# Performance work log

Measured on AMD Instinct MI355X. Metric: run time of the kernel, lower is better.

Reference implementation:

```python
import jax, jax.numpy as jnp
import numpy as np

B, N, IN_DIM, HID, OUT_DIM = 16, 1024, 128, 256, 1024
N_LAYERS, SCT_ORDER, GCN_ORDER = 2, 3, 1
TAU, N_ITER, NOISE_SCALE, TANH_SCALE = 0.1, 20, 0.05, 40.0


def _xavier(key, shape):
    # torch xavier_uniform_ on Linear weight [out, in]
    bound = np.sqrt(6.0 / (shape[-1] + shape[-2]))
    return jax.random.uniform(key, shape, jnp.float32, -bound, bound)


def setup_inputs() -> dict:
    key = jax.random.key(0)
    ks = jax.random.split(key, 12)
    L, H = N_LAYERS, HID
    return {
        "X": jax.random.normal(ks[0], (B, N, IN_DIM), jnp.float32),
        "adj": jax.random.uniform(ks[1], (B, N, N), jnp.float32),
        "w_in": _xavier(ks[2], (H, IN_DIM)),
        "b_in": jnp.zeros((H,), jnp.float32),
        "conv_w1": _xavier(ks[3], (L, H, H)),
        "conv_b1": jnp.zeros((L, H), jnp.float32),
        "conv_w2": _xavier(ks[4], (L, H, H)),
        "conv_b2": jnp.zeros((L, H), jnp.float32),
        "conv_a": 0.1 * jax.random.normal(ks[5], (L, 2 * H, 1), jnp.float32),
        "mlp1_w": _xavier(ks[6], (H, H * (1 + L))),
        "mlp1_b": jnp.zeros((H,), jnp.float32),
        "mlp2_w": _xavier(ks[7], (OUT_DIM, H)),
        "mlp2_b": jnp.zeros((OUT_DIM,), jnp.float32),
    }


def leaky(x):
    return jax.nn.leaky_relu(x, 0.01)


def gcn_diffusion(adj, order, X):
    eye = jnp.eye(adj.shape[-1], dtype=adj.dtype)
    A = adj + eye
    dis = A.sum(-1) ** -0.5                      # [B,N]
    A_hat = dis[..., :, None] * A * dis[..., None, :]
    outs, h = [], X
    for _ in range(order):
        h = A_hat @ h
        outs.append(h)
    return outs


def scattering_diffusion(adj, X, order):
    # lazy random walk P = (I + D^{-1} A)/2; wavelets psi_k = P^{2^{k-1}} - P^{2^k}
    Pmat = adj / adj.sum(-1, keepdims=True)

    def applyP(h):
        return 0.5 * (h + Pmat @ h)

    outs = []
    prev = X
    cur = applyP(X)
    outs.append(prev - cur)
    for k in range(2, order + 1):
        nxt = cur
        for _ in range(2 ** (k - 2)):
            nxt = applyP(nxt)
        outs.append(cur - nxt)
        cur = nxt
    return outs


def sct_conv(X, adj, w1, b1, w2, b2, a, moment=1):
    gcn_list = [leaky(g) for g in gcn_diffusion(adj, GCN_ORDER, X)]
    sct_list = [jnp.abs(h) ** moment for h in scattering_diffusion(adj, X, SCT_ORDER)]
    h_all = jnp.stack(gcn_list + sct_list, axis=1)                    # [B,C,N,H]
    x_rep = jnp.broadcast_to(X[:, None], h_all.shape)                 # [B,C,N,H]
    a_in = jnp.concatenate([x_rep, h_all], axis=-1)                   # [B,C,N,2H]
    e = (jax.nn.relu(a_in) @ a)[..., 0]                               # [B,C,N]
    attention = jax.nn.softmax(e + 1e-10, axis=1)[..., None]          # [B,C,N,1]
    h_prime = (attention * h_all).mean(axis=1)                        # [B,N,H]
    h = leaky(h_prime @ w1.T + b1)
    return leaky(h @ w2.T + b2)


def gumbel_sinkhorn(log_alpha, key):
    u = jax.random.uniform(key, log_alpha.shape, log_alpha.dtype)
    noise = -jnp.log(-jnp.log(u + 1e-20) + 1e-20) * NOISE_SCALE
    Z0 = (log_alpha + noise) / TAU

    def step(Z, _):
        Z = Z - jax.scipy.special.logsumexp(Z, axis=-1, keepdims=True)
        Z = Z - jax.scipy.special.logsumexp(Z, axis=-2, keepdims=True)
        return Z, None

    Z, _ = jax.lax.scan(step, Z0, None, length=N_ITER)
    P = jnp.exp(Z)
    P = P / P.sum(-1, keepdims=True)
    P = P / P.sum(-2, keepdims=True)
    return P, Z0


def reference(X, adj, w_in, b_in, conv_w1, conv_b1, conv_w2, conv_b2, conv_a,
              mlp1_w, mlp1_b, mlp2_w, mlp2_b):
    h = X @ w_in.T + b_in                                             # [B,N,H]
    hidden = [h]
    for l in range(N_LAYERS):
        h = sct_conv(h, adj, conv_w1[l], conv_b1[l], conv_w2[l], conv_b2[l], conv_a[l])
        hidden.append(h)
    h = jnp.concatenate(hidden, axis=-1)                              # [B,N,H*(1+L)]
    h = leaky(h @ mlp1_w.T + mlp1_b)
    logits = jnp.tanh(h @ mlp2_w.T + mlp2_b) * TANH_SCALE             # [B,N,N]
    P, gsinit = gumbel_sinkhorn(logits, jax.random.key(42))
    return P, gsinit
```

## Files before the change

kernel.cpp:

```cpp
#include <hip/hip_runtime.h>
#include <cstdint>
#include <cstddef>

#define BB 16
#define NN 1024
#define HD 256
#define IND 128
#define OUTD 1024
#define MROWS (BB*NN)

#define LEAKY(x) ((x) >= 0.0f ? (x) : 0.01f*(x))

typedef short short8 __attribute__((ext_vector_type(8)));
typedef float f32x4 __attribute__((ext_vector_type(4)));

#define GLL16(gsrc, ldst) __builtin_amdgcn_global_load_lds( \
    (const __attribute__((address_space(1))) unsigned int*)(gsrc), \
    (__attribute__((address_space(3))) unsigned int*)(ldst), 16, 0, 0)

#define CFENCE() asm volatile("" ::: "memory")

__device__ inline float wave_sum(float v){
  #pragma unroll
  for (int off=32; off; off>>=1) v += __shfl_xor(v, off, 64);
  return v;
}
__device__ inline float wave_max(float v){
  #pragma unroll
  for (int off=32; off; off>>=1) v = fmaxf(v, __shfl_xor(v, off, 64));
  return v;
}

__device__ inline unsigned short f2bf(float x){
  unsigned u = __float_as_uint(x);
  unsigned r = (u + 0x7fffu + ((u >> 16) & 1u)) >> 16;
  return (unsigned short)r;
}
__device__ inline float bf2f(unsigned short h){
  return __uint_as_float((unsigned)h << 16);
}

__device__ inline unsigned enc_e(float x){
  unsigned u = __float_as_uint(x);
  u += 0xFFFFFu + ((u>>20)&1u);
  int E = (int)(u>>23) - 112;
  if (E <= 0){
    unsigned Ms = (unsigned)__float2int_rn(x * 131072.0f);
    return (Ms >= 8u) ? 8u : Ms;
  }
  return ((unsigned)E<<3) | ((u>>20)&7u);
}
__device__ inline float dec_e(unsigned k){
  unsigned E = k>>3, M = k&7u;
  float nrm = __uint_as_float(((E+112u)<<23)|(M<<20));
  return E ? nrm : (float)M * 7.62939453125e-6f;
}

__device__ inline float gumbel_noise(unsigned m){
  const unsigned k0 = 0u, k1 = 42u;
  const unsigned ks2 = k0 ^ k1 ^ 0x1BD11BDAu;
  unsigned x0 = 0u, x1 = m;
  x0 += k0; x1 += k1;
  #define TF_ROUND(r) { x0 += x1; x1 = (x1 << (r)) | (x1 >> (32-(r))); x1 ^= x0; }
  TF_ROUND(13) TF_ROUND(15) TF_ROUND(26) TF_ROUND(6)
  x0 += k1;  x1 += ks2 + 1u;
  TF_ROUND(17) TF_ROUND(29) TF_ROUND(16) TF_ROUND(24)
  x0 += ks2; x1 += k0 + 2u;
  TF_ROUND(13) TF_ROUND(15) TF_ROUND(26) TF_ROUND(6)
  x0 += k0;  x1 += k1 + 3u;
  TF_ROUND(17) TF_ROUND(29) TF_ROUND(16) TF_ROUND(24)
  x0 += k1;  x1 += ks2 + 4u;
  TF_ROUND(13) TF_ROUND(15) TF_ROUND(26) TF_ROUND(6)
  x0 += ks2; x1 += k0 + 5u;
  #undef TF_ROUND
  unsigned bits = x0 ^ x1;
  float u = __uint_as_float((bits >> 9) | 0x3f800000u) - 1.0f;
  float t = -__logf(u + 1e-20f);
  return -__logf(t + 1e-20f) * 0.05f;
}

__global__ __launch_bounds__(256) void adj_prep_k(const float* __restrict__ adj,
                                                  float* __restrict__ dis,
                                                  float* __restrict__ rinv,
                                                  unsigned short* __restrict__ abf){
  int tid = threadIdx.x, wid = tid >> 6, lane = tid & 63;
  int row = blockIdx.x*4 + wid;
  const float4* rp = (const float4*)(adj + (size_t)row*NN);
  ushort4* op = (ushort4*)(abf + (size_t)row*NN);
  float s = 0.f;
  #pragma unroll
  for (int p=0;p<4;p++){
    float4 v = rp[lane + p*64];
    s += v.x+v.y+v.z+v.w;
    ushort4 o;
    o.x = f2bf(v.x); o.y = f2bf(v.y); o.z = f2bf(v.z); o.w = f2bf(v.w);
    op[lane + p*64] = o;
  }
  s = wave_sum(s);
  if (lane==0){
    dis[row]  = 1.0f/sqrtf(s + 1.0f);
    rinv[row] = 1.0f/s;
  }
}

__global__ __launch_bounds__(256) void split_flat_k(const float* __restrict__ src,
                                                    unsigned short* __restrict__ h,
                                                    unsigned short* __restrict__ l,
                                                    int n4){
  int gid = blockIdx.x*256 + threadIdx.x;
  if (gid >= n4) return;
  float4 v = ((const float4*)src)[gid];
  ushort4 hh, ll;
  hh.x = f2bf(v.x); ll.x = f2bf(v.x - bf2f(hh.x));
  hh.y = f2bf(v.y); ll.y = f2bf(v.y - bf2f(hh.y));
  hh.z = f2bf(v.z); ll.z = f2bf(v.z - bf2f(hh.z));
  hh.w = f2bf(v.w); ll.w = f2bf(v.w - bf2f(hh.w));
  ((ushort4*)h)[gid] = hh;
  ((ushort4*)l)[gid] = ll;
}

__global__ __launch_bounds__(256) void bconv_t_k(const float* __restrict__ in, int ld,
                                                 const float* __restrict__ scale,
                                                 unsigned short* __restrict__ outT){
  __shared__ float tile[64][68];
  int b  = blockIdx.z;
  int i0 = blockIdx.x*64;
  int c0 = blockIdx.y*64;
  const float* inb = in + (size_t)b*NN*ld;
  unsigned short* ob = outT + (size_t)b*HD*NN;
  int tid = threadIdx.x;
  #pragma unroll
  for (int it=0; it<4; it++){
    int f = tid + it*256;
    int r = f >> 4, c4 = (f & 15)*4;
    float4 v = *(const float4*)(inb + (size_t)(i0+r)*ld + c0 + c4);
    float s = scale ? scale[b*NN + i0 + r] : 1.0f;
    tile[r][c4+0]=v.x*s; tile[r][c4+1]=v.y*s; tile[r][c4+2]=v.z*s; tile[r][c4+3]=v.w*s;
  }
  __syncthreads();
  #pragma unroll
  for (int it=0; it<4; it++){
    int f = tid + it*256;
    int cl = f >> 4, r4 = (f & 15)*4;
    ushort4 o;
    o.x = f2bf(tile[r4+0][cl]);
    o.y = f2bf(tile[r4+1][cl]);
    o.z = f2bf(tile[r4+2][cl]);
    o.w = f2bf(tile[r4+3][cl]);
    *(ushort4*)(ob + (size_t)(c0+cl)*NN + i0 + r4) = o;
  }
}

__global__ __launch_bounds__(512) void gemm_nn_mfma_k(const unsigned short* __restrict__ Abf,
                                                      const unsigned short* __restrict__ Btb,
                                                      const float* __restrict__ Bsrc, int ldb,
                                                      const float* __restrict__ rowscale,
                                                      float* __restrict__ out,
                                                      float* __restrict__ out2,
                                                      const float* __restrict__ sub,
                                                      int mode){
  __shared__ unsigned short Als[2][128][32];
  __shared__ unsigned short Bls[2][128][32];
  int s = blockIdx.x + (blockIdx.y<<1) + (blockIdx.z<<4);
  int idx = (s&7)*32 + (s>>3);
  int b  = idx >> 4;
  int i0 = ((idx>>1)&7)*128;
  int n0 = (idx&1)*128;
  const unsigned short* Ab = Abf + (size_t)b*NN*NN + (size_t)i0*NN;
  const unsigned short* Bb = Btb + (size_t)b*HD*NN + (size_t)n0*NN;
  int tid = threadIdx.x;
  int wave = tid >> 6, lane = tid & 63;
  int quad = lane >> 4, l16 = lane & 15;
  int wr = (wave >> 2)*64;
  int wc = (wave & 3)*32;

  int r  = tid >> 2;
  int cg = (((tid & 3) ^ ((r >> 1) & 3)) << 3);
  int wbase = (tid >> 6) << 9;
  const unsigned short* gA = Ab + (size_t)r*NN + cg;
  const unsigned short* gB = Bb + (size_t)r*NN + cg;

  auto STAGE = [&](int c){
    int buf = c & 1;
    GLL16(gA + (c<<5), &Als[buf][0][0] + wbase);
    GLL16(gB + (c<<5), &Bls[buf][0][0] + wbase);
  };

  const int NC = NN/32;
  STAGE(0);

  f32x4 acc[4][2] = {};

  for (int c = 0; c < NC; ++c){
    if (c+1 < NC){
      STAGE(c+1);
      asm volatile("s_waitcnt vmcnt(2)" ::: "memory");
    } else {
      asm volatile("s_waitcnt vmcnt(0)" ::: "memory");
    }
    __builtin_amdgcn_s_barrier();
    CFENCE();
    int buf = c & 1;
    short8 af[4];
    #pragma unroll
    for (int rt=0; rt<4; rt++){
      int R = wr + rt*16 + l16;
      af[rt] = *(const short8*)&Als[buf][R][(quad ^ ((R >> 1) & 3)) << 3];
    }
    __builtin_amdgcn_s_setprio(1);
    #pragma unroll
    for (int ct=0; ct<2; ct++){
      int Rb = wc + ct*16 + l16;
      short8 bfr = *(const short8*)&Bls[buf][Rb][(quad ^ ((Rb >> 1) & 3)) << 3];
      #pragma unroll
      for (int rt=0; rt<4; rt++)
        acc[rt][ct] = __builtin_amdgcn_mfma_f32_16x16x32_bf16(af[rt], bfr, acc[rt][ct], 0, 0, 0);
    }
    __builtin_amdgcn_s_setprio(0);
    CFENCE();
    __builtin_amdgcn_s_barrier();
    CFENCE();
  }

  #pragma unroll
  for (int rt=0; rt<4; rt++){
    #pragma unroll
    for (int p=0; p<4; p++){
      int gr = i0 + wr + rt*16 + quad*4 + p;
      int gm = b*NN + gr;
      float sc = rowscale[gm];
      #pragma unroll
      for (int ct=0; ct<2; ct++){
        int gc = n0 + wc + ct*16 + l16;
        float a = acc[rt][ct][p];
        float src = Bsrc[(size_t)gm*ldb + gc];
        float o = (mode == 1) ? 0.5f*(src + sc*a) : LEAKY(sc*(a + sc*src));
        if (out) out[(size_t)gm*HD + gc] = o;
        if (out2){
          float sv = sub ? sub[(size_t)gm*HD + gc] : src;
          out2[(size_t)gm*HD + gc] = fabsf(sv - o);
        }
      }
    }
  }
}

__global__ __launch_bounds__(512) void gemm_nt_mfma_k(const unsigned short* __restrict__ Ah_,
                                                      const unsigned short* __restrict__ Al_,
                                                      int lda,
                                                      const unsigned short* __restrict__ Wh_,
                                                      const unsigned short* __restrict__ Wl_,
                                                      const float* __restrict__ bias,
                                                      float* __restrict__ out, int ldo,
                                                      unsigned short* __restrict__ outh,
                                                      unsigned short* __restrict__ outl,
                                                      int K, int act){
  __shared__ unsigned short AhL[2][128][32], AlL[2][128][32];
  __shared__ unsigned short WhL[2][128][32], WlL[2][128][32];
  int gx = gridDim.x;
  int sh = (gx == 2) ? 1 : 3;
  int s = blockIdx.x + blockIdx.y*gx;
  int nwg = gx*gridDim.y;
  int idx = (s&7)*(nwg>>3) + (s>>3);
  int o0 = (idx & (gx-1))*128;
  int m0 = (idx >> sh)*128;
  int tid = threadIdx.x;
  int wave = tid >> 6, lane = tid & 63;
  int quad = lane >> 4, l16 = lane & 15;
  int wr = (wave >> 2)*64;
  int wc = (wave & 3)*32;

  int r  = tid >> 2;
  int cg = (((tid & 3) ^ ((r >> 1) & 3)) << 3);
  int wbase = (tid >> 6) << 9;
  const unsigned short* gAh = Ah_ + (size_t)(m0 + r)*lda + cg;
  const unsigned short* gAl = Al_ + (size_t)(m0 + r)*lda + cg;
  const unsigned short* gWh = Wh_ + (size_t)(o0 + r)*K + cg;
  const unsigned short* gWl = Wl_ + (size_t)(o0 + r)*K + cg;

  int NC = K >> 5;

  auto STAGE = [&](int c){
    int buf = c & 1; int kc = c << 5;
    GLL16(gAh + kc, &AhL[buf][0][0] + wbase);
    GLL16(gAl + kc, &AlL[buf][0][0] + wbase);
    GLL16(gWh + kc, &WhL[buf][0][0] + wbase);
    GLL16(gWl + kc, &WlL[buf][0][0] + wbase);
  };

  STAGE(0);

  f32x4 acc[4][2] = {};

  for (int c = 0; c < NC; ++c){
    if (c+1 < NC){
      STAGE(c+1);
      asm volatile("s_waitcnt vmcnt(4)" ::: "memory");
    } else {
      asm volatile("s_waitcnt vmcnt(0)" ::: "memory");
    }
    __builtin_amdgcn_s_barrier();
    CFENCE();
    int buf = c & 1;
    short8 ah[4], al[4];
    #pragma unroll
    for (int rt=0; rt<4; rt++){
      int R = wr + rt*16 + l16;
      int sc = (quad ^ ((R >> 1) & 3)) << 3;
      ah[rt] = *(const short8*)&AhL[buf][R][sc];
      al[rt] = *(const short8*)&AlL[buf][R][sc];
    }
    __builtin_amdgcn_s_setprio(1);
    #pragma unroll
    for (int ct=0; ct<2; ct++){
      int Rb = wc + ct*16 + l16;
      int sc = (quad ^ ((Rb >> 1) & 3)) << 3;
      short8 wh = *(const short8*)&WhL[buf][Rb][sc];
      short8 wl = *(const short8*)&WlL[buf][Rb][sc];
      #pragma unroll
      for (int rt=0; rt<4; rt++){
        acc[rt][ct] = __builtin_amdgcn_mfma_f32_16x16x32_bf16(ah[rt], wh, acc[rt][ct], 0, 0, 0);
        acc[rt][ct] = __builtin_amdgcn_mfma_f32_16x16x32_bf16(al[rt], wh, acc[rt][ct], 0, 0, 0);
        acc[rt][ct] = __builtin_amdgcn_mfma_f32_16x16x32_bf16(ah[rt], wl, acc[rt][ct], 0, 0, 0);
      }
    }
    __builtin_amdgcn_s_setprio(0);
    CFENCE();
    __builtin_amdgcn_s_barrier();
    CFENCE();
  }

  #pragma unroll
  for (int rt=0; rt<4; rt++){
    #pragma unroll
    for (int p=0; p<4; p++){
      int gm = m0 + wr + rt*16 + quad*4 + p;
      #pragma unroll
      for (int ct=0; ct<2; ct++){
        int gc = o0 + wc + ct*16 + l16;
        float v = acc[rt][ct][p] + bias[gc];
        if (act == 1){
          v = LEAKY(v);
        } else if (act == 2){
          float vcl = fminf(fmaxf(v, -15.f), 15.f);
          float e = __expf(2.f*vcl);
          float lg = 40.0f * (e - 1.f) / (e + 1.f);
          unsigned flat = (unsigned)gm*1024u + (unsigned)gc;
          v = (lg + gumbel_noise(flat)) / 0.1f;
        }
        if (out) out[(size_t)gm*ldo + gc] = v;
        if (outh){
          unsigned short hh = f2bf(v);
          outh[(size_t)gm*ldo + gc] = hh;
          outl[(size_t)gm*ldo + gc] = f2bf(v - bf2f(hh));
        }
      }
    }
  }
}

__global__ __launch_bounds__(256) void attn_k(const float* __restrict__ c0,
                                              const float* __restrict__ s0,
                                              const float* __restrict__ s1,
                                              const float* __restrict__ s2,
                                              const float* __restrict__ a2,
                                              unsigned short* __restrict__ outh,
                                              unsigned short* __restrict__ outl){
  int tid = threadIdx.x, wid = tid >> 6, lane = tid & 63;
  int row = blockIdx.x*4 + wid;
  size_t base = (size_t)row*HD + lane*4;
  float4 av = *(const float4*)(a2 + lane*4);
  float4 v[4];
  v[0] = *(const float4*)(c0 + base);
  v[1] = *(const float4*)(s0 + base);
  v[2] = *(const float4*)(s1 + base);
  v[3] = *(const float4*)(s2 + base);
  float e[4];
  #pragma unroll
  for (int c=0;c<4;c++){
    float p = fmaxf(v[c].x,0.f)*av.x + fmaxf(v[c].y,0.f)*av.y
            + fmaxf(v[c].z,0.f)*av.z + fmaxf(v[c].w,0.f)*av.w;
    e[c] = wave_sum(p);
  }
  float m = fmaxf(fmaxf(e[0],e[1]), fmaxf(e[2],e[3]));
  float w0 = expf(e[0]-m), w1 = expf(e[1]-m), w2 = expf(e[2]-m), w3 = expf(e[3]-m);
  float inv = 0.25f / (w0+w1+w2+w3);
  float4 o;
  o.x = (w0*v[0].x + w1*v[1].x + w2*v[2].x + w3*v[3].x)*inv;
  o.y = (w0*v[0].y + w1*v[1].y + w2*v[2].y + w3*v[3].y)*inv;
  o.z = (w0*v[0].z + w1*v[1].z + w2*v[2].z + w3*v[3].z)*inv;
  o.w = (w0*v[0].w + w1*v[1].w + w2*v[2].w + w3*v[3].w)*inv;
  ushort4 oh, ol;
  oh.x = f2bf(o.x); ol.x = f2bf(o.x - bf2f(oh.x));
  oh.y = f2bf(o.y); ol.y = f2bf(o.y - bf2f(oh.y));
  oh.z = f2bf(o.z); ol.z = f2bf(o.z - bf2f(oh.z));
  oh.w = f2bf(o.w); ol.w = f2bf(o.w - bf2f(oh.w));
  *(ushort4*)(outh + base) = oh;
  *(ushort4*)(outl + base) = ol;
}

__global__ __launch_bounds__(256) void rowmax_k(const float* __restrict__ Z,
                                                float* __restrict__ alpha){
  int tid = threadIdx.x, wid = tid >> 6, lane = tid & 63;
  int row = blockIdx.x*4 + wid;
  const float4* rp = (const float4*)(Z + (size_t)row*NN);
  float m = -3.4e38f;
  #pragma unroll
  for (int p=0;p<4;p++){
    float4 v = rp[lane + p*64];
    m = fmaxf(m, fmaxf(fmaxf(v.x,v.y), fmaxf(v.z,v.w)));
  }
  m = wave_max(m);
  if (lane==0) alpha[row] = m;
}

__global__ __launch_bounds__(256) void colmax_k(const float* __restrict__ Z,
                                                const float* __restrict__ alpha,
                                                float* __restrict__ pmax){
  int b = blockIdx.y, rc = blockIdx.x;
  int j = threadIdx.x*4;
  const float* Zb = Z + (size_t)b*NN*NN;
  const float* ab = alpha + b*NN;
  float4 m = make_float4(-3.4e38f,-3.4e38f,-3.4e38f,-3.4e38f);
  int r0 = rc*32;
  #pragma unroll 4
  for (int r=r0; r<r0+32; r++){
    float4 v = *(const float4*)(Zb + (size_t)r*NN + j);
    float a = ab[r];
    m.x = fmaxf(m.x, v.x-a); m.y = fmaxf(m.y, v.y-a);
    m.z = fmaxf(m.z, v.z-a); m.w = fmaxf(m.w, v.w-a);
  }
  *(float4*)(pmax + ((size_t)b*32 + rc)*NN + j) = m;
}

__global__ __launch_bounds__(256) void colred_k(const float* __restrict__ pmax,
                                                float* __restrict__ beta){
  int b = blockIdx.y;
  int j = blockIdx.x*256 + threadIdx.x;
  float m = -3.4e38f;
  #pragma unroll
  for (int rc=0; rc<32; rc++)
    m = fmaxf(m, pmax[((size_t)b*32+rc)*NN + j]);
  beta[b*NN + j] = m;
}

__global__ __launch_bounds__(256) void build_e_k(const float* __restrict__ Z,
                                                 const float* __restrict__ alpha,
                                                 const float* __restrict__ beta,
                                                 unsigned char* __restrict__ E,
                                                 unsigned char* __restrict__ Et){
  __shared__ float tile[64][65];
  int b = blockIdx.z;
  int i0 = blockIdx.y*64, j0 = blockIdx.x*64;
  const float* Zb = Z + (size_t)b*NN*NN;
  const float* ab = alpha + b*NN;
  const float* bb = beta  + b*NN;
  unsigned char* Eb  = E  + (size_t)b*NN*NN;
  unsigned char* Etb = Et + (size_t)b*NN*NN;
  int tid = threadIdx.x;
  #pragma unroll
  for (int it=0; it<4; it++){
    int f = tid + it*256;
    int r = f >> 4, c4 = (f & 15)*4;
    float4 v = *(const float4*)(Zb + (size_t)(i0+r)*NN + j0 + c4);
    float a = ab[i0+r];
    float e0 = __expf(v.x - a - bb[j0+c4+0]);
    float e1 = __expf(v.y - a - bb[j0+c4+1]);
    float e2 = __expf(v.z - a - bb[j0+c4+2]);
    float e3 = __expf(v.w - a - bb[j0+c4+3]);
    tile[r][c4+0]=e0; tile[r][c4+1]=e1; tile[r][c4+2]=e2; tile[r][c4+3]=e3;
    uchar4 o;
    o.x=(unsigned char)enc_e(e0); o.y=(unsigned char)enc_e(e1);
    o.z=(unsigned char)enc_e(e2); o.w=(unsigned char)enc_e(e3);
    *(uchar4*)(Eb + (size_t)(i0+r)*NN + j0 + c4) = o;
  }
  __syncthreads();
  #pragma unroll
  for (int it=0; it<4; it++){
    int f = tid + it*256;
    int r = f >> 4, c4 = (f & 15)*4;
    uchar4 o;
    o.x = (unsigned char)enc_e(tile[c4+0][r]);
    o.y = (unsigned char)enc_e(tile[c4+1][r]);
    o.z = (unsigned char)enc_e(tile[c4+2][r]);
    o.w = (unsigned char)enc_e(tile[c4+3][r]);
    *(uchar4*)(Etb + (size_t)(j0+r)*NN + i0 + c4) = o;
  }
}

__global__ __launch_bounds__(256) void mv_k(const unsigned char* __restrict__ M,
                                            const float* __restrict__ v,
                                            float* __restrict__ w, int recip){
  int tid = threadIdx.x, wid = tid >> 6, lane = tid & 63;
  int row = blockIdx.x*4 + wid;
  int b = row >> 10;
  uint4 mw = *((const uint4*)(M + (size_t)row*NN) + lane);
  float s = 0.f;
  if (v){
    const float* vb = v + b*NN + lane*16;
    float4 v0 = *(const float4*)(vb);
    float4 v1 = *(const float4*)(vb+4);
    float4 v2 = *(const float4*)(vb+8);
    float4 v3 = *(const float4*)(vb+12);
    s += dec_e(mw.x&255u)*v0.x + dec_e((mw.x>>8)&255u)*v0.y
       + dec_e((mw.x>>16)&255u)*v0.z + dec_e(mw.x>>24)*v0.w;
    s += dec_e(mw.y&255u)*v1.x + dec_e((mw.y>>8)&255u)*v1.y
       + dec_e((mw.y>>16)&255u)*v1.z + dec_e(mw.y>>24)*v1.w;
    s += dec_e(mw.z&255u)*v2.x + dec_e((mw.z>>8)&255u)*v2.y
       + dec_e((mw.z>>16)&255u)*v2.z + dec_e(mw.z>>24)*v2.w;
    s += dec_e(mw.w&255u)*v3.x + dec_e((mw.w>>8)&255u)*v3.y
       + dec_e((mw.w>>16)&255u)*v3.z + dec_e(mw.w>>24)*v3.w;
  } else {
    s += dec_e(mw.x&255u) + dec_e((mw.x>>8)&255u) + dec_e((mw.x>>16)&255u) + dec_e(mw.x>>24);
    s += dec_e(mw.y&255u) + dec_e((mw.y>>8)&255u) + dec_e((mw.y>>16)&255u) + dec_e(mw.y>>24);
    s += dec_e(mw.z&255u) + dec_e((mw.z>>8)&255u) + dec_e((mw.z>>16)&255u) + dec_e(mw.z>>24);
    s += dec_e(mw.w&255u) + dec_e((mw.w>>8)&255u) + dec_e((mw.w>>16)&255u) + dec_e(mw.w>>24);
  }
  s = wave_sum(s);
  if (lane==0) w[row] = recip ? 1.0f/s : s;
}

__global__ __launch_bounds__(256) void writep_lin_k(const unsigned char* __restrict__ E,
                                                    const float* __restrict__ ap,
                                                    const float* __restrict__ tp,
                                                    float* __restrict__ P){
  int gid = blockIdx.x*256 + threadIdx.x;
  int row = gid >> 8;
  int j = (gid & 255)*4;
  int b = row >> 10;
  uchar4 e = ((const uchar4*)E)[gid];
  float a = ap[row];
  float4 t = *(const float4*)(tp + (size_t)b*NN + j);
  float4 o;
  o.x = dec_e(e.x)*a/t.x;
  o.y = dec_e(e.y)*a/t.y;
  o.z = dec_e(e.z)*a/t.z;
  o.w = dec_e(e.w)*a/t.w;
  ((float4*)P)[gid] = o;
}

extern "C" void kernel_launch(void* const* d_in, const int* in_sizes, int n_in,
                              void* d_out, int out_size, void* d_ws, size_t ws_size,
                              hipStream_t stream){
  const float* X    = (const float*)d_in[0];
  const float* adj  = (const float*)d_in[1];
  const float* w_in = (const float*)d_in[2];
  const float* b_in = (const float*)d_in[3];
  const float* cw1  = (const float*)d_in[4];
  const float* cb1  = (const float*)d_in[5];
  const float* cw2  = (const float*)d_in[6];
  const float* cb2  = (const float*)d_in[7];
  const float* ca   = (const float*)d_in[8];
  const float* m1w  = (const float*)d_in[9];
  const float* m1b  = (const float*)d_in[10];
  const float* m2w  = (const float*)d_in[11];
  const float* m2b  = (const float*)d_in[12];

  float* outp = (float*)d_out;
  float* Pout = outp;
  float* Z0   = outp + (size_t)16*1024*1024;

  const size_t SLOT = (size_t)4*1024*1024;
  float* s1 = outp + 0*SLOT;
  float* s2 = outp + 1*SLOT;
  float* s3 = outp + 2*SLOT;
  float* s4 = outp + 3*SLOT;
  float* s5 = outp + 4*SLOT;
  unsigned short* adjbf = (unsigned short*)(outp + 6*SLOT);

  unsigned short* Xh  = (unsigned short*)(outp + 0*SLOT);
  unsigned short* Xl  = Xh + (size_t)MROWS*IND;
  unsigned short* s4h = (unsigned short*)(outp + 3*SLOT);
  unsigned short* s4l = s4h + (size_t)MROWS*HD;
  unsigned short* l1h = (unsigned short*)(outp + 0*SLOT);
  unsigned short* l1l = l1h + (size_t)MROWS*HD;
  unsigned short* m1sh = (unsigned short*)(outp + 1*SLOT);
  unsigned short* m1sl = m1sh + (size_t)MROWS*HD;
  unsigned short* Hh = (unsigned short*)(outp + 2*SLOT);
  unsigned short* Hl = Hh + (size_t)MROWS*768;
  float* alpha = s1;
  float* beta  = s1 + 16384;
  float* pmaxb = s1 + 32768;

  float* ws     = (float*)d_ws;
  float* hidden = ws;
  float* dis    = ws + (size_t)12*1024*1024;
  float* rinv   = dis + 16384;
  unsigned short* bt = (unsigned short*)(rinv + 16384);
  unsigned short* wsp = (unsigned short*)(ws + (size_t)15*1024*1024);
  unsigned short* winh = wsp;               unsigned short* winl = winh + 32768;
  unsigned short* w1h  = winl + 32768;      unsigned short* w1l  = w1h + 131072;
  unsigned short* w2h  = w1l + 131072;      unsigned short* w2l  = w2h + 131072;
  unsigned short* m1h  = w2l + 131072;      unsigned short* m1l  = m1h + 196608;
  unsigned short* m2h  = m1l + 196608;      unsigned short* m2l  = m2h + 262144;
  unsigned char* E  = (unsigned char*)ws;
  unsigned char* Et = E + (size_t)MROWS*NN;
  float* av = ws + (size_t)16*1024*1024;
  float* bv = av + 16384;
  float* tv = bv + 16384;

  dim3 blk(256);
  dim3 gEw(4096);
  dim3 gMM(2, 8, 16);
  dim3 gCT(16, 4, 16);

  adj_prep_k<<<gEw, blk, 0, stream>>>(adj, dis, rinv, adjbf);
  split_flat_k<<<dim3(32),  blk, 0, stream>>>(w_in, winh, winl, 8192);
  split_flat_k<<<dim3(128), blk, 0, stream>>>(cw1,  w1h,  w1l,  32768);
  split_flat_k<<<dim3(128), blk, 0, stream>>>(cw2,  w2h,  w2l,  32768);
  split_flat_k<<<dim3(192), blk, 0, stream>>>(m1w,  m1h,  m1l,  49152);
  split_flat_k<<<dim3(256), blk, 0, stream>>>(m2w,  m2h,  m2l,  65536);
  split_flat_k<<<dim3(2048), blk, 0, stream>>>(X, Xh, Xl, 524288);

  gemm_nt_mfma_k<<<dim3(2,128), dim3(512), 0, stream>>>(Xh, Xl, IND,
                                                        winh, winl, b_in,
                                                        hidden, 768, nullptr, nullptr,
                                                        IND, 0);

  for (int l=0; l<2; l++){
    const float* h_in = hidden + l*HD;
    unsigned short* wl1h = w1h + (size_t)l*65536;
    unsigned short* wl1l = w1l + (size_t)l*65536;
    unsigned short* wl2h = w2h + (size_t)l*65536;
    unsigned short* wl2l = w2l + (size_t)l*65536;
    const float* b1 = cb1 + (size_t)l*HD;
    const float* b2 = cb2 + (size_t)l*HD;
    const float* a2 = ca  + (size_t)l*2*HD + HD;

    bconv_t_k<<<gCT, blk, 0, stream>>>(h_in, 768, dis, bt);
    gemm_nn_mfma_k<<<gMM, dim3(512), 0, stream>>>(adjbf, bt, h_in, 768, dis, s2, nullptr, nullptr, 2);
    bconv_t_k<<<gCT, blk, 0, stream>>>(h_in, 768, nullptr, bt);
    gemm_nn_mfma_k<<<gMM, dim3(512), 0, stream>>>(adjbf, bt, h_in, 768, rinv, s1, s3, nullptr, 1);
    bconv_t_k<<<gCT, blk, 0, stream>>>(s1, HD, nullptr, bt);
    gemm_nn_mfma_k<<<gMM, dim3(512), 0, stream>>>(adjbf, bt, s1, HD, rinv, s4, s5, nullptr, 1);
    bconv_t_k<<<gCT, blk, 0, stream>>>(s4, HD, nullptr, bt);
    gemm_nn_mfma_k<<<gMM, dim3(512), 0, stream>>>(adjbf, bt, s4, HD, rinv, s1, nullptr, nullptr, 1);
    bconv_t_k<<<gCT, blk, 0, stream>>>(s1, HD, nullptr, bt);
    gemm_nn_mfma_k<<<gMM, dim3(512), 0, stream>>>(adjbf, bt, s1, HD, rinv, nullptr, s1, s4, 1);
    attn_k<<<gEw, blk, 0, stream>>>(s2, s3, s5, s1, a2, s4h, s4l);
    gemm_nt_mfma_k<<<dim3(2,128), dim3(512), 0, stream>>>(s4h, s4l, HD,
                                                          wl1h, wl1l, b1,
                                                          nullptr, HD, l1h, l1l,
                                                          HD, 1);
    gemm_nt_mfma_k<<<dim3(2,128), dim3(512), 0, stream>>>(l1h, l1l, HD,
                                                          wl2h, wl2l, b2,
                                                          hidden + (l+1)*HD, 768,
                                                          nullptr, nullptr, HD, 1);
  }

  split_flat_k<<<dim3(12288), blk, 0, stream>>>(hidden, Hh, Hl, 3145728);
  gemm_nt_mfma_k<<<dim3(2,128), dim3(512), 0, stream>>>(Hh, Hl, 768,
                                                        m1h, m1l, m1b,
                                                        nullptr, HD, m1sh, m1sl,
                                                        768, 1);
  gemm_nt_mfma_k<<<dim3(8,128), dim3(512), 0, stream>>>(m1sh, m1sl, HD,
                                                        m2h, m2l, m2b,
                                                        Z0, OUTD, nullptr, nullptr,
                                                        HD, 2);

  rowmax_k<<<gEw, blk, 0, stream>>>(Z0, alpha);
  colmax_k<<<dim3(32,16), blk, 0, stream>>>(Z0, alpha, pmaxb);
  colred_k<<<dim3(4,16), blk, 0, stream>>>(pmaxb, beta);
  build_e_k<<<dim3(16,16,16), blk, 0, stream>>>(Z0, alpha, beta, E, Et);

  mv_k<<<gEw, blk, 0, stream>>>(E,  nullptr, av, 1);
  mv_k<<<gEw, blk, 0, stream>>>(Et, av,      bv, 1);
  for (int t=1; t<20; t++){
    mv_k<<<gEw, blk, 0, stream>>>(E,  bv, av, 1);
    mv_k<<<gEw, blk, 0, stream>>>(Et, av, bv, 1);
  }
  mv_k<<<gEw, blk, 0, stream>>>(E,  bv, av, 1);
  mv_k<<<gEw, blk, 0, stream>>>(Et, av, tv, 0);
  writep_lin_k<<<dim3(16384), blk, 0, stream>>>(E, av, tv, Pout);
}
```

Baseline: 1.216 ms.

## Fuse Sinkhorn iterations into persistent kernel with grid barrier; deepen GEMM pipeline

```diff
diff --git a/kernel.cpp b/kernel.cpp
--- a/kernel.cpp
+++ b/kernel.cpp
@@ -8,6 +8,7 @@
 #define IND 128
 #define OUTD 1024
 #define MROWS (BB*NN)
+#define NBLK 256
 
 #define LEAKY(x) ((x) >= 0.0f ? (x) : 0.01f*(x))
 
@@ -42,18 +43,31 @@
 
 __device__ inline unsigned enc_e(float x){
   unsigned u = __float_as_uint(x);
-  u += 0xFFFFFu + ((u>>20)&1u);
-  int E = (int)(u>>23) - 112;
-  if (E <= 0){
-    unsigned Ms = (unsigned)__float2int_rn(x * 131072.0f);
-    return (Ms >= 8u) ? 8u : Ms;
-  }
-  return ((unsigned)E<<3) | ((u>>20)&7u);
+  u += 0x7FFFFu + ((u>>20)&1u);
+  unsigned e = u>>23;
+  if (e < 97u) return 0u;
+  return ((e-96u)<<3) | ((u>>20)&7u);
 }
 __device__ inline float dec_e(unsigned k){
-  unsigned E = k>>3, M = k&7u;
-  float nrm = __uint_as_float(((E+112u)<<23)|(M<<20));
-  return E ? nrm : (float)M * 7.62939453125e-6f;
+  float nrm = __uint_as_float((k + 768u) << 20);
+  return k ? nrm : 0.0f;
+}
+
+__device__ inline void gsync(unsigned* bar){
+  asm volatile("s_waitcnt vmcnt(0)" ::: "memory");
+  __syncthreads();
+  if (threadIdx.x == 0){
+    unsigned g = __hip_atomic_load(&bar[1], __ATOMIC_RELAXED, __HIP_MEMORY_SCOPE_AGENT);
+    unsigned o = __hip_atomic_fetch_add(&bar[0], 1u, __ATOMIC_RELAXED, __HIP_MEMORY_SCOPE_AGENT);
+    if (o == NBLK-1u){
+      __hip_atomic_store(&bar[0], 0u, __ATOMIC_RELAXED, __HIP_MEMORY_SCOPE_AGENT);
+      __hip_atomic_fetch_add(&bar[1], 1u, __ATOMIC_RELEASE, __HIP_MEMORY_SCOPE_AGENT);
+    } else {
+      while (__hip_atomic_load(&bar[1], __ATOMIC_RELAXED, __HIP_MEMORY_SCOPE_AGENT) == g)
+        __builtin_amdgcn_s_sleep(16);
+    }
+  }
+  __syncthreads();
 }
 
 __device__ inline float gumbel_noise(unsigned m){
@@ -159,8 +173,8 @@
                                                       float* __restrict__ out2,
                                                       const float* __restrict__ sub,
                                                       int mode){
-  __shared__ unsigned short Als[2][128][32];
-  __shared__ unsigned short Bls[2][128][32];
+  __shared__ unsigned short Als[4][128][32];
+  __shared__ unsigned short Bls[4][128][32];
   int s = blockIdx.x + (blockIdx.y<<1) + (blockIdx.z<<4);
   int idx = (s&7)*32 + (s>>3);
   int b  = idx >> 4;
@@ -180,27 +194,29 @@
   const unsigned short* gA = Ab + (size_t)r*NN + cg;
   const unsigned short* gB = Bb + (size_t)r*NN + cg;
 
-  auto STAGE = [&](int c){
-    int buf = c & 1;
-    GLL16(gA + (c<<5), &Als[buf][0][0] + wbase);
-    GLL16(gB + (c<<5), &Bls[buf][0][0] + wbase);
+  auto STAGE = [&](int t){
+    int buf = t & 3;
+    GLL16(gA + (t<<5), &Als[buf][0][0] + wbase);
+    GLL16(gB + (t<<5), &Bls[buf][0][0] + wbase);
   };
 
-  const int NC = NN/32;
-  STAGE(0);
+  const int NT = NN/32;
+  STAGE(0); STAGE(1);
 
   f32x4 acc[4][2] = {};
 
-  for (int c = 0; c < NC; ++c){
-    if (c+1 < NC){
-      STAGE(c+1);
+  for (int t = 0; t < NT; ++t){
+    if (t+2 < NT){
+      STAGE(t+2);
+      asm volatile("s_waitcnt vmcnt(4)" ::: "memory");
+    } else if (t+1 < NT){
       asm volatile("s_waitcnt vmcnt(2)" ::: "memory");
     } else {
       asm volatile("s_waitcnt vmcnt(0)" ::: "memory");
     }
     __builtin_amdgcn_s_barrier();
     CFENCE();
-    int buf = c & 1;
+    int buf = t & 3;
     short8 af[4];
     #pragma unroll
     for (int rt=0; rt<4; rt++){
@@ -217,9 +233,6 @@
         acc[rt][ct] = __builtin_amdgcn_mfma_f32_16x16x32_bf16(af[rt], bfr, acc[rt][ct], 0, 0, 0);
     }
     __builtin_amdgcn_s_setprio(0);
-    CFENCE();
-    __builtin_amdgcn_s_barrier();
-    CFENCE();
   }
 
   #pragma unroll
@@ -399,38 +412,37 @@
   *(ushort4*)(outl + base) = ol;
 }
 
-__global__ __launch_bounds__(256) void rowmax_k(const float* __restrict__ Z,
-                                                float* __restrict__ alpha){
+__global__ __launch_bounds__(256) void rowcolmax_k(const float* __restrict__ Z,
+                                                   float* __restrict__ alpha,
+                                                   float* __restrict__ pmax){
+  __shared__ float al[64];
   int tid = threadIdx.x, wid = tid >> 6, lane = tid & 63;
-  int row = blockIdx.x*4 + wid;
-  const float4* rp = (const float4*)(Z + (size_t)row*NN);
-  float m = -3.4e38f;
-  #pragma unroll
-  for (int p=0;p<4;p++){
-    float4 v = rp[lane + p*64];
-    m = fmaxf(m, fmaxf(fmaxf(v.x,v.y), fmaxf(v.z,v.w)));
-  }
-  m = wave_max(m);
-  if (lane==0) alpha[row] = m;
-}
-
-__global__ __launch_bounds__(256) void colmax_k(const float* __restrict__ Z,
-                                                const float* __restrict__ alpha,
-                                                float* __restrict__ pmax){
-  int b = blockIdx.y, rc = blockIdx.x;
-  int j = threadIdx.x*4;
-  const float* Zb = Z + (size_t)b*NN*NN;
-  const float* ab = alpha + b*NN;
-  float4 m = make_float4(-3.4e38f,-3.4e38f,-3.4e38f,-3.4e38f);
-  int r0 = rc*32;
+  int blk = blockIdx.x;
+  int r0 = blk << 6;
+  #pragma unroll 1
+  for (int rr=0; rr<16; ++rr){
+    int lr = (wid<<4) + rr;
+    const float4* rp = (const float4*)(Z + ((size_t)(r0+lr)<<10));
+    float m = -3.4e38f;
+    #pragma unroll
+    for (int p4=0;p4<4;p4++){
+      float4 v = rp[lane + p4*64];
+      m = fmaxf(m, fmaxf(fmaxf(v.x,v.y), fmaxf(v.z,v.w)));
+    }
+    m = wave_max(m);
+    if (lane==0){ al[lr] = m; alpha[r0+lr] = m; }
+  }
+  __syncthreads();
+  int j = tid*4;
+  float4 mm = make_float4(-3.4e38f,-3.4e38f,-3.4e38f,-3.4e38f);
   #pragma unroll 4
-  for (int r=r0; r<r0+32; r++){
-    float4 v = *(const float4*)(Zb + (size_t)r*NN + j);
-    float a = ab[r];
-    m.x = fmaxf(m.x, v.x-a); m.y = fmaxf(m.y, v.y-a);
-    m.z = fmaxf(m.z, v.z-a); m.w = fmaxf(m.w, v.w-a);
-  }
-  *(float4*)(pmax + ((size_t)b*32 + rc)*NN + j) = m;
+  for (int rr=0; rr<64; ++rr){
+    float4 v = *(const float4*)(Z + ((size_t)(r0+rr)<<10) + j);
+    float a = al[rr];
+    mm.x = fmaxf(mm.x, v.x-a); mm.y = fmaxf(mm.y, v.y-a);
+    mm.z = fmaxf(mm.z, v.z-a); mm.w = fmaxf(mm.w, v.w-a);
+  }
+  *(float4*)(pmax + ((size_t)blk<<10) + j) = mm;
 }
 
 __global__ __launch_bounds__(256) void colred_k(const float* __restrict__ pmax,
@@ -439,8 +451,8 @@
   int j = blockIdx.x*256 + threadIdx.x;
   float m = -3.4e38f;
   #pragma unroll
-  for (int rc=0; rc<32; rc++)
-    m = fmaxf(m, pmax[((size_t)b*32+rc)*NN + j]);
+  for (int rc=0; rc<16; rc++)
+    m = fmaxf(m, pmax[((size_t)(b*16+rc)<<10) + j]);
   beta[b*NN + j] = m;
 }
 
@@ -488,55 +500,87 @@
   }
 }
 
-__global__ __launch_bounds__(256) void mv_k(const unsigned char* __restrict__ M,
-                                            const float* __restrict__ v,
-                                            float* __restrict__ w, int recip){
+__global__ __launch_bounds__(256, 1) void sinkhorn_pers_k(const unsigned char* __restrict__ E,
+                                                          const unsigned char* __restrict__ Et,
+                                                          float* __restrict__ av,
+                                                          float* __restrict__ bv,
+                                                          float* __restrict__ tv,
+                                                          unsigned* __restrict__ bar,
+                                                          float* __restrict__ P){
   int tid = threadIdx.x, wid = tid >> 6, lane = tid & 63;
-  int row = blockIdx.x*4 + wid;
-  int b = row >> 10;
-  uint4 mw = *((const uint4*)(M + (size_t)row*NN) + lane);
-  float s = 0.f;
-  if (v){
-    const float* vb = v + b*NN + lane*16;
-    float4 v0 = *(const float4*)(vb);
-    float4 v1 = *(const float4*)(vb+4);
-    float4 v2 = *(const float4*)(vb+8);
-    float4 v3 = *(const float4*)(vb+12);
-    s += dec_e(mw.x&255u)*v0.x + dec_e((mw.x>>8)&255u)*v0.y
-       + dec_e((mw.x>>16)&255u)*v0.z + dec_e(mw.x>>24)*v0.w;
-    s += dec_e(mw.y&255u)*v1.x + dec_e((mw.y>>8)&255u)*v1.y
-       + dec_e((mw.y>>16)&255u)*v1.z + dec_e(mw.y>>24)*v1.w;
-    s += dec_e(mw.z&255u)*v2.x + dec_e((mw.z>>8)&255u)*v2.y
-       + dec_e((mw.z>>16)&255u)*v2.z + dec_e(mw.z>>24)*v2.w;
-    s += dec_e(mw.w&255u)*v3.x + dec_e((mw.w>>8)&255u)*v3.y
-       + dec_e((mw.w>>16)&255u)*v3.z + dec_e(mw.w>>24)*v3.w;
-  } else {
-    s += dec_e(mw.x&255u) + dec_e((mw.x>>8)&255u) + dec_e((mw.x>>16)&255u) + dec_e(mw.x>>24);
-    s += dec_e(mw.y&255u) + dec_e((mw.y>>8)&255u) + dec_e((mw.y>>16)&255u) + dec_e(mw.y>>24);
-    s += dec_e(mw.z&255u) + dec_e((mw.z>>8)&255u) + dec_e((mw.z>>16)&255u) + dec_e(mw.z>>24);
-    s += dec_e(mw.w&255u) + dec_e((mw.w>>8)&255u) + dec_e((mw.w>>16)&255u) + dec_e(mw.w>>24);
-  }
-  s = wave_sum(s);
-  if (lane==0) w[row] = recip ? 1.0f/s : s;
-}
-
-__global__ __launch_bounds__(256) void writep_lin_k(const unsigned char* __restrict__ E,
-                                                    const float* __restrict__ ap,
-                                                    const float* __restrict__ tp,
-                                                    float* __restrict__ P){
-  int gid = blockIdx.x*256 + threadIdx.x;
-  int row = gid >> 8;
-  int j = (gid & 255)*4;
-  int b = row >> 10;
-  uchar4 e = ((const uchar4*)E)[gid];
-  float a = ap[row];
-  float4 t = *(const float4*)(tp + (size_t)b*NN + j);
-  float4 o;
-  o.x = dec_e(e.x)*a/t.x;
-  o.y = dec_e(e.y)*a/t.y;
-  o.z = dec_e(e.z)*a/t.z;
-  o.w = dec_e(e.w)*a/t.w;
-  ((float4*)P)[gid] = o;
+  int blk = blockIdx.x;
+  int r0 = blk << 6;
+  int vbase = (r0 >> 10) << 10;
+
+  float vreg[16];
+  #pragma unroll
+  for (int q=0;q<16;q++) vreg[q] = 1.0f;
+
+  #define DECSUM(mwp, base) ( \
+      dec_e( (mwp)      &255u)*vreg[base+0] + dec_e(((mwp)>>8 )&255u)*vreg[base+1] + \
+      dec_e(((mwp)>>16) &255u)*vreg[base+2] + dec_e( (mwp)>>24       )*vreg[base+3] )
+
+  for (int p = 0; p < 42; ++p){
+    const unsigned char* M = (p & 1) ? Et : E;
+    float* wout = (p & 1) ? ((p == 41) ? tv : bv) : av;
+    int recip = (p != 41);
+    #pragma unroll 1
+    for (int rr=0; rr<16; ++rr){
+      int row = r0 + (wid<<4) + rr;
+      uint4 mw = *((const uint4*)(M + ((size_t)row<<10)) + lane);
+      float s = DECSUM(mw.x,0) + DECSUM(mw.y,4) + DECSUM(mw.z,8) + DECSUM(mw.w,12);
+      s = wave_sum(s);
+      if (lane==0){
+        float o = recip ? 1.0f/s : s;
+        __hip_atomic_store(&wout[row], o, __ATOMIC_RELAXED, __HIP_MEMORY_SCOPE_AGENT);
+      }
+    }
+    gsync(bar);
+    if (p < 41){
+      const float* vin = (p & 1) ? bv : av;
+      #pragma unroll
+      for (int q=0;q<16;q++)
+        vreg[q] = __hip_atomic_load(&vin[vbase + lane*16 + q],
+                                    __ATOMIC_RELAXED, __HIP_MEMORY_SCOPE_AGENT);
+    }
+  }
+  #undef DECSUM
+
+  float tinv[16];
+  #pragma unroll
+  for (int q=0;q<16;q++){
+    float t = __hip_atomic_load(&tv[vbase + lane*16 + q],
+                                __ATOMIC_RELAXED, __HIP_MEMORY_SCOPE_AGENT);
+    tinv[q] = 1.0f/t;
+  }
+  #pragma unroll 1
+  for (int rr=0; rr<16; ++rr){
+    int row = r0 + (wid<<4) + rr;
+    float a = __hip_atomic_load(&av[row], __ATOMIC_RELAXED, __HIP_MEMORY_SCOPE_AGENT);
+    uint4 mw = *((const uint4*)(E + ((size_t)row<<10)) + lane);
+    float* Pr = P + ((size_t)row<<10) + lane*16;
+    float4 o;
+    o.x = dec_e( mw.x      &255u)*a*tinv[0];
+    o.y = dec_e((mw.x>>8 ) &255u)*a*tinv[1];
+    o.z = dec_e((mw.x>>16) &255u)*a*tinv[2];
+    o.w = dec_e( mw.x>>24        )*a*tinv[3];
+    *(float4*)(Pr+0) = o;
+    o.x = dec_e( mw.y      &255u)*a*tinv[4];
+    o.y = dec_e((mw.y>>8 ) &255u)*a*tinv[5];
+    o.z = dec_e((mw.y>>16) &255u)*a*tinv[6];
+    o.w = dec_e( mw.y>>24        )*a*tinv[7];
+    *(float4*)(Pr+4) = o;
+    o.x = dec_e( mw.z      &255u)*a*tinv[8];
+    o.y = dec_e((mw.z>>8 ) &255u)*a*tinv[9];
+    o.z = dec_e((mw.z>>16) &255u)*a*tinv[10];
+    o.w = dec_e( mw.z>>24        )*a*tinv[11];
+    *(float4*)(Pr+8) = o;
+    o.x = dec_e( mw.w      &255u)*a*tinv[12];
+    o.y = dec_e((mw.w>>8 ) &255u)*a*tinv[13];
+    o.z = dec_e((mw.w>>16) &255u)*a*tinv[14];
+    o.w = dec_e( mw.w>>24        )*a*tinv[15];
+    *(float4*)(Pr+12) = o;
+  }
 }
 
 extern "C" void kernel_launch(void* const* d_in, const int* in_sizes, int n_in,
@@ -598,6 +642,7 @@
   float* av = ws + (size_t)16*1024*1024;
   float* bv = av + 16384;
   float* tv = bv + 16384;
+  unsigned* bar = (unsigned*)(tv + 16384);
 
   dim3 blk(256);
   dim3 gEw(4096);
@@ -658,18 +703,9 @@
                                                         Z0, OUTD, nullptr, nullptr,
                                                         HD, 2);
 
-  rowmax_k<<<gEw, blk, 0, stream>>>(Z0, alpha);
-  colmax_k<<<dim3(32,16), blk, 0, stream>>>(Z0, alpha, pmaxb);
+  rowcolmax_k<<<dim3(256), blk, 0, stream>>>(Z0, alpha, pmaxb);
   colred_k<<<dim3(4,16), blk, 0, stream>>>(pmaxb, beta);
   build_e_k<<<dim3(16,16,16), blk, 0, stream>>>(Z0, alpha, beta, E, Et);
-
-  mv_k<<<gEw, blk, 0, stream>>>(E,  nullptr, av, 1);
-  mv_k<<<gEw, blk, 0, stream>>>(Et, av,      bv, 1);
-  for (int t=1; t<20; t++){
-    mv_k<<<gEw, blk, 0, stream>>>(E,  bv, av, 1);
-    mv_k<<<gEw, blk, 0, stream>>>(Et, av, bv, 1);
-  }
-  mv_k<<<gEw, blk, 0, stream>>>(E,  bv, av, 1);
-  mv_k<<<gEw, blk, 0, stream>>>(Et, av, tv, 0);
-  writep_lin_k<<<dim3(16384), blk, 0, stream>>>(E, av, tv, Pout);
-}
+  hipMemsetAsync(bar, 0, 2*sizeof(unsigned), stream);
+  sinkhorn_pers_k<<<dim3(NBLK), blk, 0, stream>>>(E, Et, av, bv, tv, bar, Pout);
+}
```

New measurement: 1.773 ms. +45.8%, slower.

## Deepen GEMM prefetch, fuse transpose conversions and row/col max, change E encoding

Applied to the files above, without the earlier changes.

```diff
diff --git a/kernel.cpp b/kernel.cpp
--- a/kernel.cpp
+++ b/kernel.cpp
@@ -42,18 +42,14 @@
 
 __device__ inline unsigned enc_e(float x){
   unsigned u = __float_as_uint(x);
-  u += 0xFFFFFu + ((u>>20)&1u);
-  int E = (int)(u>>23) - 112;
-  if (E <= 0){
-    unsigned Ms = (unsigned)__float2int_rn(x * 131072.0f);
-    return (Ms >= 8u) ? 8u : Ms;
-  }
-  return ((unsigned)E<<3) | ((u>>20)&7u);
+  u += 0x7FFFFu + ((u>>20)&1u);
+  unsigned e = u>>23;
+  if (e < 97u) return 0u;
+  return ((e-96u)<<3) | ((u>>20)&7u);
 }
 __device__ inline float dec_e(unsigned k){
-  unsigned E = k>>3, M = k&7u;
-  float nrm = __uint_as_float(((E+112u)<<23)|(M<<20));
-  return E ? nrm : (float)M * 7.62939453125e-6f;
+  float nrm = __uint_as_float((k + 768u) << 20);
+  return k ? nrm : 0.0f;
 }
 
 __device__ inline float gumbel_noise(unsigned m){
@@ -151,6 +147,44 @@
   }
 }
 
+__global__ __launch_bounds__(256) void bconv2_t_k(const float* __restrict__ in, int ld,
+                                                  const float* __restrict__ scale,
+                                                  unsigned short* __restrict__ outS,
+                                                  unsigned short* __restrict__ outP){
+  __shared__ float tile[64][68];
+  __shared__ float srow[64];
+  int b  = blockIdx.z;
+  int i0 = blockIdx.x*64;
+  int c0 = blockIdx.y*64;
+  const float* inb = in + (size_t)b*NN*ld;
+  unsigned short* obS = outS + (size_t)b*HD*NN;
+  unsigned short* obP = outP + (size_t)b*HD*NN;
+  int tid = threadIdx.x;
+  if (tid < 64) srow[tid] = scale[b*NN + i0 + tid];
+  #pragma unroll
+  for (int it=0; it<4; it++){
+    int f = tid + it*256;
+    int r = f >> 4, c4 = (f & 15)*4;
+    float4 v = *(const float4*)(inb + (size_t)(i0+r)*ld + c0 + c4);
+    tile[r][c4+0]=v.x; tile[r][c4+1]=v.y; tile[r][c4+2]=v.z; tile[r][c4+3]=v.w;
+  }
+  __syncthreads();
+  #pragma unroll
+  for (int it=0; it<4; it++){
+    int f = tid + it*256;
+    int cl = f >> 4, r4 = (f & 15)*4;
+    float t0 = tile[r4+0][cl], t1 = tile[r4+1][cl];
+    float t2 = tile[r4+2][cl], t3 = tile[r4+3][cl];
+    ushort4 p, s;
+    p.x = f2bf(t0); p.y = f2bf(t1); p.z = f2bf(t2); p.w = f2bf(t3);
+    s.x = f2bf(t0*srow[r4+0]); s.y = f2bf(t1*srow[r4+1]);
+    s.z = f2bf(t2*srow[r4+2]); s.w = f2bf(t3*srow[r4+3]);
+    size_t off = (size_t)(c0+cl)*NN + i0 + r4;
+    *(ushort4*)(obP + off) = p;
+    *(ushort4*)(obS + off) = s;
+  }
+}
+
 __global__ __launch_bounds__(512) void gemm_nn_mfma_k(const unsigned short* __restrict__ Abf,
                                                       const unsigned short* __restrict__ Btb,
                                                       const float* __restrict__ Bsrc, int ldb,
@@ -159,8 +193,8 @@
                                                       float* __restrict__ out2,
                                                       const float* __restrict__ sub,
                                                       int mode){
-  __shared__ unsigned short Als[2][128][32];
-  __shared__ unsigned short Bls[2][128][32];
+  __shared__ unsigned short Als[4][128][32];
+  __shared__ unsigned short Bls[4][128][32];
   int s = blockIdx.x + (blockIdx.y<<1) + (blockIdx.z<<4);
   int idx = (s&7)*32 + (s>>3);
   int b  = idx >> 4;
@@ -180,27 +214,29 @@
   const unsigned short* gA = Ab + (size_t)r*NN + cg;
   const unsigned short* gB = Bb + (size_t)r*NN + cg;
 
-  auto STAGE = [&](int c){
-    int buf = c & 1;
-    GLL16(gA + (c<<5), &Als[buf][0][0] + wbase);
-    GLL16(gB + (c<<5), &Bls[buf][0][0] + wbase);
+  auto STAGE = [&](int t){
+    int buf = t & 3;
+    GLL16(gA + (t<<5), &Als[buf][0][0] + wbase);
+    GLL16(gB + (t<<5), &Bls[buf][0][0] + wbase);
   };
 
-  const int NC = NN/32;
-  STAGE(0);
+  const int NT = NN/32;
+  STAGE(0); STAGE(1);
 
   f32x4 acc[4][2] = {};
 
-  for (int c = 0; c < NC; ++c){
-    if (c+1 < NC){
-      STAGE(c+1);
+  for (int t = 0; t < NT; ++t){
+    if (t+2 < NT){
+      STAGE(t+2);
+      asm volatile("s_waitcnt vmcnt(4)" ::: "memory");
+    } else if (t+1 < NT){
       asm volatile("s_waitcnt vmcnt(2)" ::: "memory");
     } else {
       asm volatile("s_waitcnt vmcnt(0)" ::: "memory");
     }
     __builtin_amdgcn_s_barrier();
     CFENCE();
-    int buf = c & 1;
+    int buf = t & 3;
     short8 af[4];
     #pragma unroll
     for (int rt=0; rt<4; rt++){
@@ -217,9 +253,6 @@
         acc[rt][ct] = __builtin_amdgcn_mfma_f32_16x16x32_bf16(af[rt], bfr, acc[rt][ct], 0, 0, 0);
     }
     __builtin_amdgcn_s_setprio(0);
-    CFENCE();
-    __builtin_amdgcn_s_barrier();
-    CFENCE();
   }
 
   #pragma unroll
@@ -399,38 +432,37 @@
   *(ushort4*)(outl + base) = ol;
 }
 
-__global__ __launch_bounds__(256) void rowmax_k(const float* __restrict__ Z,
-                                                float* __restrict__ alpha){
+__global__ __launch_bounds__(256) void rowcolmax_k(const float* __restrict__ Z,
+                                                   float* __restrict__ alpha,
+                                                   float* __restrict__ pmax){
+  __shared__ float al[64];
   int tid = threadIdx.x, wid = tid >> 6, lane = tid & 63;
-  int row = blockIdx.x*4 + wid;
-  const float4* rp = (const float4*)(Z + (size_t)row*NN);
-  float m = -3.4e38f;
-  #pragma unroll
-  for (int p=0;p<4;p++){
-    float4 v = rp[lane + p*64];
-    m = fmaxf(m, fmaxf(fmaxf(v.x,v.y), fmaxf(v.z,v.w)));
-  }
-  m = wave_max(m);
-  if (lane==0) alpha[row] = m;
-}
-
-__global__ __launch_bounds__(256) void colmax_k(const float* __restrict__ Z,
-                                                const float* __restrict__ alpha,
-                                                float* __restrict__ pmax){
-  int b = blockIdx.y, rc = blockIdx.x;
-  int j = threadIdx.x*4;
-  const float* Zb = Z + (size_t)b*NN*NN;
-  const float* ab = alpha + b*NN;
-  float4 m = make_float4(-3.4e38f,-3.4e38f,-3.4e38f,-3.4e38f);
-  int r0 = rc*32;
+  int blk = blockIdx.x;
+  int r0 = blk << 6;
+  #pragma unroll 1
+  for (int rr=0; rr<16; ++rr){
+    int lr = (wid<<4) + rr;
+    const float4* rp = (const float4*)(Z + ((size_t)(r0+lr)<<10));
+    float m = -3.4e38f;
+    #pragma unroll
+    for (int p4=0;p4<4;p4++){
+      float4 v = rp[lane + p4*64];
+      m = fmaxf(m, fmaxf(fmaxf(v.x,v.y), fmaxf(v.z,v.w)));
+    }
+    m = wave_max(m);
+    if (lane==0){ al[lr] = m; alpha[r0+lr] = m; }
+  }
+  __syncthreads();
+  int j = tid*4;
+  float4 mm = make_float4(-3.4e38f,-3.4e38f,-3.4e38f,-3.4e38f);
   #pragma unroll 4
-  for (int r=r0; r<r0+32; r++){
-    float4 v = *(const float4*)(Zb + (size_t)r*NN + j);
-    float a = ab[r];
-    m.x = fmaxf(m.x, v.x-a); m.y = fmaxf(m.y, v.y-a);
-    m.z = fmaxf(m.z, v.z-a); m.w = fmaxf(m.w, v.w-a);
-  }
-  *(float4*)(pmax + ((size_t)b*32 + rc)*NN + j) = m;
+  for (int rr=0; rr<64; ++rr){
+    float4 v = *(const float4*)(Z + ((size_t)(r0+rr)<<10) + j);
+    float a = al[rr];
+    mm.x = fmaxf(mm.x, v.x-a); mm.y = fmaxf(mm.y, v.y-a);
+    mm.z = fmaxf(mm.z, v.z-a); mm.w = fmaxf(mm.w, v.w-a);
+  }
+  *(float4*)(pmax + ((size_t)blk<<10) + j) = mm;
 }
 
 __global__ __launch_bounds__(256) void colred_k(const float* __restrict__ pmax,
@@ -439,8 +471,8 @@
   int j = blockIdx.x*256 + threadIdx.x;
   float m = -3.4e38f;
   #pragma unroll
-  for (int rc=0; rc<32; rc++)
-    m = fmaxf(m, pmax[((size_t)b*32+rc)*NN + j]);
+  for (int rc=0; rc<16; rc++)
+    m = fmaxf(m, pmax[((size_t)(b*16+rc)<<10) + j]);
   beta[b*NN + j] = m;
 }
 
@@ -566,6 +598,7 @@
   float* s3 = outp + 2*SLOT;
   float* s4 = outp + 3*SLOT;
   float* s5 = outp + 4*SLOT;
+  unsigned short* bt2   = (unsigned short*)(outp + 5*SLOT);
   unsigned short* adjbf = (unsigned short*)(outp + 6*SLOT);
 
   unsigned short* Xh  = (unsigned short*)(outp + 0*SLOT);
@@ -627,10 +660,9 @@
     const float* b2 = cb2 + (size_t)l*HD;
     const float* a2 = ca  + (size_t)l*2*HD + HD;
 
-    bconv_t_k<<<gCT, blk, 0, stream>>>(h_in, 768, dis, bt);
+    bconv2_t_k<<<gCT, blk, 0, stream>>>(h_in, 768, dis, bt, bt2);
     gemm_nn_mfma_k<<<gMM, dim3(512), 0, stream>>>(adjbf, bt, h_in, 768, dis, s2, nullptr, nullptr, 2);
-    bconv_t_k<<<gCT, blk, 0, stream>>>(h_in, 768, nullptr, bt);
-    gemm_nn_mfma_k<<<gMM, dim3(512), 0, stream>>>(adjbf, bt, h_in, 768, rinv, s1, s3, nullptr, 1);
+    gemm_nn_mfma_k<<<gMM, dim3(512), 0, stream>>>(adjbf, bt2, h_in, 768, rinv, s1, s3, nullptr, 1);
     bconv_t_k<<<gCT, blk, 0, stream>>>(s1, HD, nullptr, bt);
     gemm_nn_mfma_k<<<gMM, dim3(512), 0, stream>>>(adjbf, bt, s1, HD, rinv, s4, s5, nullptr, 1);
     bconv_t_k<<<gCT, blk, 0, stream>>>(s4, HD, nullptr, bt);
@@ -658,8 +690,7 @@
                                                         Z0, OUTD, nullptr, nullptr,
                                                         HD, 2);
 
-  rowmax_k<<<gEw, blk, 0, stream>>>(Z0, alpha);
-  colmax_k<<<dim3(32,16), blk, 0, stream>>>(Z0, alpha, pmaxb);
+  rowcolmax_k<<<dim3(256), blk, 0, stream>>>(Z0, alpha, pmaxb);
   colred_k<<<dim3(4,16), blk, 0, stream>>>(pmaxb, beta);
   build_e_k<<<dim3(16,16,16), blk, 0, stream>>>(Z0, alpha, beta, E, Et);
 
```

Measured after the change: 1.110 ms. 1.1x faster.
